# Kernel tuning notes

Hardware: AMD Instinct MI355X
Metric: run time of the kernel (lower is better)

Reference implementation:

```python
import jax, jax.numpy as jnp
import numpy as np

B, CIN, HID, COUT, D, L = 2, 32, 64, 32, 20, 3
D2 = 2 * D
C4, C2 = COUT // 4, COUT // 2


def _conv3(x, W, b):
    # dense stride-1 'SAME' conv == MinkowskiConvolution on occupied set (background is 0)
    y = jax.lax.conv_general_dilated(x, W, (1, 1, 1), 'SAME',
                                     dimension_numbers=('NCDHW', 'OIDHW', 'NCDHW'))
    return y + b[None, :, None, None, None]


def _up(x, W, b):
    # generative conv-transpose, kernel 2 stride 2: out[:, :, 2i+p, 2j+q, 2k+r] = sum_c W[c,:,p,q,r] x[:,c,i,j,k]
    y = jnp.einsum('bcxyz,cdpqr->bdxpyqzr', x, W)
    y = y.reshape(x.shape[0], W.shape[1], 2 * x.shape[2], 2 * x.shape[3], 2 * x.shape[4])
    return y + b[None, :, None, None, None]


def _forward(x_feat, x_occ, target_occ, W_up, b_up, W_conv, b_conv,
             blk_W00, blk_b00, blk_W01, blk_b01, blk_W10, blk_b10,
             blk_W11, blk_b11, blk_W12, blk_b12, W_cls, b_cls, adaptive, rho=1.0):
    b = x_feat.shape[0]
    # occupancy of upsampled coords: every input voxel spawns its 2x2x2 children
    occ_up = jnp.repeat(jnp.repeat(jnp.repeat(x_occ, 2, 1), 2, 2), 2, 3)  # [B,D2,D2,D2]
    m = occ_up[:, None].astype(x_feat.dtype)
    out = jax.nn.relu(_up(x_feat, W_up, b_up) * m)
    out = jax.nn.relu(_conv3(out, W_conv, b_conv) * m)
    # InceptionResNet blocks (PCGCv2 style): two branches, concat, residual add
    for i in range(L):
        o0 = jax.nn.relu(_conv3(out, blk_W00[i], blk_b00[i]) * m)
        o0 = _conv3(o0, blk_W01[i], blk_b01[i]) * m
        o1 = jax.nn.relu(_conv3(out, blk_W10[i], blk_b10[i]) * m)
        o1 = jax.nn.relu(_conv3(o1, blk_W11[i], blk_b11[i]) * m)
        o1 = _conv3(o1, blk_W12[i], blk_b12[i]) * m
        out = jnp.concatenate([o0, o1], axis=1) + out
    out_cls = _conv3(out, W_cls, b_cls) * m
    # get_target_by_sp_tensor: isin(out coords, target coords) -> dense mask intersection
    occ_b = occ_up.astype(bool)
    target = occ_b & target_occ.astype(bool)
    # keep mask (computed under no_grad in torch)
    cls = jax.lax.stop_gradient(out_cls[:, 0]).reshape(b, -1)
    occ_flat = occ_b.reshape(b, -1)
    if adaptive:
        vals = jnp.where(occ_flat, cls, -jnp.inf)
        t_cnt = target_occ.astype(bool).reshape(b, -1).sum(-1)
        k = jnp.minimum(occ_flat.sum(-1), (t_cnt.astype(jnp.float32) * rho).astype(jnp.int32))
        order = jnp.argsort(-vals, axis=-1)
        ranks = jnp.argsort(order, axis=-1)   # descending rank of each voxel
        keep = (ranks < k[:, None]) & occ_flat
    else:
        keep = (cls > 0) & occ_flat
    keep = keep.reshape(occ_b.shape)
    keep = keep | target  # training mode: keep += target
    out_pruned = out * keep[:, None].astype(out.dtype)
    return out_pruned, out_cls, target, keep


def setup_inputs() -> dict:
    key = jax.random.key(0)
    ks = jax.random.split(key, 12)
    s = 0.05
    occ = jax.random.randint(ks[0], (B, D, D, D), 0, 2).astype(jnp.int32)
    x_feat = jax.random.normal(ks[1], (B, CIN, D, D, D), jnp.float32) * occ[:, None].astype(jnp.float32)
    target_occ = jax.random.randint(ks[2], (B, D2, D2, D2), 0, 2).astype(jnp.int32)
    return {
        'x_feat': x_feat, 'x_occ': occ, 'target_occ': target_occ,
        'W_up': jax.random.normal(ks[3], (CIN, HID, 2, 2, 2), jnp.float32) * s,
        'b_up': jnp.zeros((HID,), jnp.float32),
        'W_conv': jax.random.normal(ks[4], (COUT, HID, 3, 3, 3), jnp.float32) * s,
        'b_conv': jnp.zeros((COUT,), jnp.float32),
        'blk_W00': jax.random.normal(ks[5], (L, C4, COUT, 3, 3, 3), jnp.float32) * s,
        'blk_b00': jnp.zeros((L, C4), jnp.float32),
        'blk_W01': jax.random.normal(ks[6], (L, C2, C4, 3, 3, 3), jnp.float32) * s,
        'blk_b01': jnp.zeros((L, C2), jnp.float32),
        'blk_W10': jax.random.normal(ks[7], (L, C4, COUT, 1, 1, 1), jnp.float32) * s,
        'blk_b10': jnp.zeros((L, C4), jnp.float32),
        'blk_W11': jax.random.normal(ks[8], (L, C4, C4, 3, 3, 3), jnp.float32) * s,
        'blk_b11': jnp.zeros((L, C4), jnp.float32),
        'blk_W12': jax.random.normal(ks[9], (L, C2, C4, 1, 1, 1), jnp.float32) * s,
        'blk_b12': jnp.zeros((L, C2), jnp.float32),
        'W_cls': jax.random.normal(ks[10], (1, COUT, 3, 3, 3), jnp.float32) * s,
        'b_cls': jnp.zeros((1,), jnp.float32),
        'adaptive': 1,
    }


def reference(x_feat, x_occ, target_occ, W_up, b_up, W_conv, b_conv,
              blk_W00, blk_b00, blk_W01, blk_b01, blk_W10, blk_b10,
              blk_W11, blk_b11, blk_W12, blk_b12, W_cls, b_cls, adaptive):
    return _forward(x_feat, x_occ, target_occ, W_up, b_up, W_conv, b_conv,
                    blk_W00, blk_b00, blk_W01, blk_b01, blk_W10, blk_b10,
                    blk_W11, blk_b11, blk_W12, blk_b12, W_cls, b_cls, adaptive)
```

## Files before the change

### kernel.cpp

```cpp
#include <hip/hip_runtime.h>
#include <hip/hip_bf16.h>

#define S3 64000
#define NB 2

constexpr int OFF_WUP   = 0;
constexpr int OFF_WCONV = 16384;
constexpr int OFF_W00   = 71680;
constexpr int OFF_W01   = 92416;
constexpr int OFF_W10   = 102784;
constexpr int OFF_W11   = 103552;
constexpr int OFF_W12   = 108736;
constexpr int OFF_ZERO  = 109120;
constexpr int OFF_WCLS  = 109184;
constexpr int NPACK     = 110048;

__device__ const int g_offtab[27] = {
  -1641, -1640, -1639, -1601, -1600, -1599, -1561, -1560, -1559,
    -41,   -40,   -39,    -1,     0,     1,    39,    40,    41,
   1559,  1560,  1561,  1599,  1600,  1601,  1639,  1640,  1641
};

__device__ __forceinline__ int occ_at(const int* __restrict__ x_occ, int b, int s) {
  int d2 = s % 40; int t = s / 40; int d1 = t % 40; int d0 = t / 40;
  return x_occ[b * 8000 + (d0 >> 1) * 400 + (d1 >> 1) * 20 + (d2 >> 1)] != 0;
}

__device__ __forceinline__ unsigned int f2key(float f) {
  unsigned int u = __float_as_uint(f);
  return (u & 0x80000000u) ? ~u : (u | 0x80000000u);
}

__device__ __forceinline__ unsigned int edge_mask27(int d0, int d1, int d2) {
  unsigned int m = 0;
  #pragma unroll
  for (int k0 = 0; k0 < 3; ++k0)
  #pragma unroll
  for (int k1 = 0; k1 < 3; ++k1)
  #pragma unroll
  for (int k2 = 0; k2 < 3; ++k2) {
    bool ok = (k0 == 0 ? (d0 > 0) : (k0 == 2 ? (d0 < 39) : true))
           && (k1 == 0 ? (d1 > 0) : (k1 == 2 ? (d1 < 39) : true))
           && (k2 == 0 ? (d2 > 0) : (k2 == 2 ? (d2 < 39) : true));
    if (ok) m |= 1u << ((k0 * 3 + k1) * 3 + k2);
  }
  return m;
}

__global__ __launch_bounds__(256)
void pack_all(const float* __restrict__ Wup, const float* __restrict__ Wconv,
              const float* __restrict__ W00, const float* __restrict__ W01,
              const float* __restrict__ W10, const float* __restrict__ W11,
              const float* __restrict__ W12, const float* __restrict__ Wcls,
              float* __restrict__ wp) {
  int i = blockIdx.x * 256 + threadIdx.x;
  if (i < 16384) {
    int tap = i >> 11, rem = i & 2047, c = rem >> 6, d = rem & 63;
    wp[OFF_WUP + i] = Wup[((c << 6) | d) * 8 + tap];
    return;
  }
  i -= 16384;
  if (i < 55296) {
    int tap = i >> 11, c = (i >> 5) & 63, co = i & 31;
    wp[OFF_WCONV + i] = Wconv[(co * 64 + c) * 27 + tap];
    return;
  }
  i -= 55296;
  if (i < 20736) {
    int blk = i / 6912, r = i - blk * 6912;
    int tap = r >> 8, c = (r >> 3) & 31, co = r & 7;
    wp[OFF_W00 + i] = W00[((blk * 8 + co) * 32 + c) * 27 + tap];
    return;
  }
  i -= 20736;
  if (i < 10368) {
    int blk = i / 3456, r = i - blk * 3456;
    int tap = r >> 7, c = (r >> 4) & 7, co = r & 15;
    wp[OFF_W01 + i] = W01[((blk * 16 + co) * 8 + c) * 27 + tap];
    return;
  }
  i -= 10368;
  if (i < 768) {
    int blk = i / 256, r = i - blk * 256;
    int c = r >> 3, co = r & 7;
    wp[OFF_W10 + i] = W10[(blk * 8 + co) * 32 + c];
    return;
  }
  i -= 768;
  if (i < 5184) {
    int blk = i / 1728, r = i - blk * 1728;
    int tap = r >> 6, c = (r >> 3) & 7, co = r & 7;
    wp[OFF_W11 + i] = W11[((blk * 8 + co) * 8 + c) * 27 + tap];
    return;
  }
  i -= 5184;
  if (i < 384) {
    int blk = i / 128, r = i - blk * 128;
    int c = r >> 4, co = r & 15;
    wp[OFF_W12 + i] = W12[(blk * 16 + co) * 8 + c];
    return;
  }
  i -= 384;
  if (i < 64) {
    wp[OFF_ZERO + i] = 0.f;
    return;
  }
  i -= 64;
  if (i < 864) {
    int tap = i / 32, c = i % 32;
    wp[OFF_WCLS + i] = Wcls[c * 27 + tap];
  }
}

__global__ __launch_bounds__(64)
void up_kernel(const float* __restrict__ xf, const float* __restrict__ wup,
               const float* __restrict__ bup, const int* __restrict__ x_occ,
               float* __restrict__ outA) {
  int pv = blockIdx.x * 64 + threadIdx.x;
  int b = pv / 8000, p = pv - b * 8000;
  int p2 = p % 20, t = p / 20, p1 = t % 20, p0 = t / 20;
  int tap = blockIdx.y;
  int O0 = 2 * p0 + (tap >> 2), O1 = 2 * p1 + ((tap >> 1) & 1), O2 = 2 * p2 + (tap & 1);
  int s = O0 * 1600 + O1 * 40 + O2;
  float* op = outA + ((size_t)b * S3 + s) * 64;
  int occ = x_occ[pv];
  float4 z4 = make_float4(0.f, 0.f, 0.f, 0.f);
  if (!occ) {
    #pragma unroll
    for (int i = 0; i < 16; ++i) ((float4*)op)[i] = z4;
    return;
  }
  float acc[64];
  #pragma unroll
  for (int d = 0; d < 64; ++d) acc[d] = bup[d];
  const float* xb = xf + (size_t)b * 32 * 8000 + p;
  const float* wt = wup + tap * 2048;
  #pragma unroll 1
  for (int c = 0; c < 32; ++c) {
    float v = xb[c * 8000];
    const float* w = wt + c * 64;
    #pragma unroll
    for (int d = 0; d < 64; ++d) acc[d] = fmaf(v, w[d], acc[d]);
  }
  #pragma unroll
  for (int i = 0; i < 16; ++i)
    ((float4*)op)[i] = make_float4(fmaxf(acc[4*i],0.f), fmaxf(acc[4*i+1],0.f),
                                   fmaxf(acc[4*i+2],0.f), fmaxf(acc[4*i+3],0.f));
}

template<int CIN, int COUT, int WS, bool RELU>
__global__ __launch_bounds__(256)
void conv3_cl(const float* __restrict__ in, const float* __restrict__ w,
              const float* __restrict__ bias, const int* __restrict__ x_occ,
              const float* __restrict__ zpage, float* __restrict__ out, int outc) {
  int tid = blockIdx.x * 256 + threadIdx.x;
  int b = tid / S3, s = tid - b * S3;
  int d2 = s % 40; int t = s / 40; int d1 = t % 40; int d0 = t / 40;
  int occ = x_occ[b * 8000 + (d0 >> 1) * 400 + (d1 >> 1) * 20 + (d2 >> 1)];
  int cb = blockIdx.y * COUT;
  float* op = out + (size_t)tid * outc + cb;
  float4 z4 = make_float4(0.f, 0.f, 0.f, 0.f);
  if (!occ) {
    #pragma unroll
    for (int i = 0; i < COUT / 4; ++i) ((float4*)op)[i] = z4;
    return;
  }
  const float* wb = w + cb;
  const float* bb = bias + cb;
  float acc[COUT];
  #pragma unroll
  for (int co = 0; co < COUT; ++co) acc[co] = bb[co];
  const float* inb = in + (size_t)tid * CIN;
  unsigned int m27 = edge_mask27(d0, d1, d2);
  #pragma unroll 1
  for (int tap = 0; tap < 27; ++tap) {
    const float* p = ((m27 >> tap) & 1) ? (inb + g_offtab[tap] * CIN) : zpage;
    const float* wt = wb + tap * CIN * WS;
    #pragma unroll
    for (int c4 = 0; c4 < CIN / 4; ++c4) {
      float4 v = ((const float4*)p)[c4];
      const float* wc = wt + c4 * 4 * WS;
      #pragma unroll
      for (int co = 0; co < COUT; ++co) acc[co] = fmaf(v.x, wc[co], acc[co]);
      #pragma unroll
      for (int co = 0; co < COUT; ++co) acc[co] = fmaf(v.y, wc[WS + co], acc[co]);
      #pragma unroll
      for (int co = 0; co < COUT; ++co) acc[co] = fmaf(v.z, wc[2 * WS + co], acc[co]);
      #pragma unroll
      for (int co = 0; co < COUT; ++co) acc[co] = fmaf(v.w, wc[3 * WS + co], acc[co]);
    }
  }
  #pragma unroll
  for (int co = 0; co < COUT; ++co) if (RELU) acc[co] = fmaxf(acc[co], 0.f);
  #pragma unroll
  for (int i = 0; i < COUT / 4; ++i)
    ((float4*)op)[i] = make_float4(acc[4*i], acc[4*i+1], acc[4*i+2], acc[4*i+3]);
}

__global__ __launch_bounds__(256)
void conv_k1(const float* __restrict__ in, const float* __restrict__ w3,
             const float* __restrict__ w1, const float* __restrict__ b3,
             const float* __restrict__ b1, const int* __restrict__ x_occ,
             const float* __restrict__ zpage, float* __restrict__ T0o,
             float* __restrict__ T1o) {
  int tid = blockIdx.x * 256 + threadIdx.x;
  int b = tid / S3, s = tid - b * S3;
  int d2 = s % 40; int t = s / 40; int d1 = t % 40; int d0 = t / 40;
  int occ = x_occ[b * 8000 + (d0 >> 1) * 400 + (d1 >> 1) * 20 + (d2 >> 1)];
  float* o0 = T0o + (size_t)tid * 8;
  float* o1 = T1o + (size_t)tid * 8;
  float4 z4 = make_float4(0.f, 0.f, 0.f, 0.f);
  if (!occ) {
    ((float4*)o0)[0] = z4; ((float4*)o0)[1] = z4;
    ((float4*)o1)[0] = z4; ((float4*)o1)[1] = z4;
    return;
  }
  float a0[8], a1[8];
  #pragma unroll
  for (int co = 0; co < 8; ++co) { a0[co] = b3[co]; a1[co] = b1[co]; }
  const float* inb = in + (size_t)tid * 32;
  #pragma unroll
  for (int c4 = 0; c4 < 8; ++c4) {
    float4 v = ((const float4*)inb)[c4];
    const float* wc = w1 + c4 * 4 * 8;
    #pragma unroll
    for (int co = 0; co < 8; ++co) a1[co] = fmaf(v.x, wc[co], a1[co]);
    #pragma unroll
    for (int co = 0; co < 8; ++co) a1[co] = fmaf(v.y, wc[8 + co], a1[co]);
    #pragma unroll
    for (int co = 0; co < 8; ++co) a1[co] = fmaf(v.z, wc[16 + co], a1[co]);
    #pragma unroll
    for (int co = 0; co < 8; ++co) a1[co] = fmaf(v.w, wc[24 + co], a1[co]);
  }
  unsigned int m27 = edge_mask27(d0, d1, d2);
  #pragma unroll 1
  for (int tap = 0; tap < 27; ++tap) {
    const float* p = ((m27 >> tap) & 1) ? (inb + g_offtab[tap] * 32) : zpage;
    const float* wt = w3 + tap * 32 * 8;
    #pragma unroll
    for (int c4 = 0; c4 < 8; ++c4) {
      float4 v = ((const float4*)p)[c4];
      const float* wc = wt + c4 * 4 * 8;
      #pragma unroll
      for (int co = 0; co < 8; ++co) a0[co] = fmaf(v.x, wc[co], a0[co]);
      #pragma unroll
      for (int co = 0; co < 8; ++co) a0[co] = fmaf(v.y, wc[8 + co], a0[co]);
      #pragma unroll
      for (int co = 0; co < 8; ++co) a0[co] = fmaf(v.z, wc[16 + co], a0[co]);
      #pragma unroll
      for (int co = 0; co < 8; ++co) a0[co] = fmaf(v.w, wc[24 + co], a0[co]);
    }
  }
  ((float4*)o0)[0] = make_float4(fmaxf(a0[0],0.f), fmaxf(a0[1],0.f), fmaxf(a0[2],0.f), fmaxf(a0[3],0.f));
  ((float4*)o0)[1] = make_float4(fmaxf(a0[4],0.f), fmaxf(a0[5],0.f), fmaxf(a0[6],0.f), fmaxf(a0[7],0.f));
  ((float4*)o1)[0] = make_float4(fmaxf(a1[0],0.f), fmaxf(a1[1],0.f), fmaxf(a1[2],0.f), fmaxf(a1[3],0.f));
  ((float4*)o1)[1] = make_float4(fmaxf(a1[4],0.f), fmaxf(a1[5],0.f), fmaxf(a1[6],0.f), fmaxf(a1[7],0.f));
}

__global__ __launch_bounds__(256)
void conv_k3(const float* __restrict__ t0, const float* __restrict__ t2,
             const float* __restrict__ resid, const float* __restrict__ w01,
             const float* __restrict__ w12, const float* __restrict__ bb01,
             const float* __restrict__ bb12, const int* __restrict__ x_occ,
             const float* __restrict__ zpage, float* __restrict__ nxt) {
  int tid = blockIdx.x * 256 + threadIdx.x;
  int b = tid / S3, s = tid - b * S3;
  int d2 = s % 40; int t = s / 40; int d1 = t % 40; int d0 = t / 40;
  int occ = x_occ[b * 8000 + (d0 >> 1) * 400 + (d1 >> 1) * 20 + (d2 >> 1)];
  float* op = nxt + (size_t)tid * 32;
  float4 z4 = make_float4(0.f, 0.f, 0.f, 0.f);
  if (!occ) {
    #pragma unroll
    for (int i = 0; i < 8; ++i) ((float4*)op)[i] = z4;
    return;
  }
  float a[32];
  #pragma unroll
  for (int co = 0; co < 16; ++co) { a[co] = bb01[co]; a[16 + co] = bb12[co]; }
  const float* t0b = t0 + (size_t)tid * 8;
  unsigned int m27 = edge_mask27(d0, d1, d2);
  #pragma unroll 1
  for (int tap = 0; tap < 27; ++tap) {
    const float* p = ((m27 >> tap) & 1) ? (t0b + g_offtab[tap] * 8) : zpage;
    const float* wt = w01 + tap * 8 * 16;
    #pragma unroll
    for (int c4 = 0; c4 < 2; ++c4) {
      float4 v = ((const float4*)p)[c4];
      const float* wc = wt + c4 * 4 * 16;
      #pragma unroll
      for (int co = 0; co < 16; ++co) a[co] = fmaf(v.x, wc[co], a[co]);
      #pragma unroll
      for (int co = 0; co < 16; ++co) a[co] = fmaf(v.y, wc[16 + co], a[co]);
      #pragma unroll
      for (int co = 0; co < 16; ++co) a[co] = fmaf(v.z, wc[32 + co], a[co]);
      #pragma unroll
      for (int co = 0; co < 16; ++co) a[co] = fmaf(v.w, wc[48 + co], a[co]);
    }
  }
  const float* t2b = t2 + (size_t)tid * 8;
  #pragma unroll
  for (int c4 = 0; c4 < 2; ++c4) {
    float4 v = ((const float4*)t2b)[c4];
    const float* wc = w12 + c4 * 4 * 16;
    #pragma unroll
    for (int co = 0; co < 16; ++co) a[16 + co] = fmaf(v.x, wc[co], a[16 + co]);
    #pragma unroll
    for (int co = 0; co < 16; ++co) a[16 + co] = fmaf(v.y, wc[16 + co], a[16 + co]);
    #pragma unroll
    for (int co = 0; co < 16; ++co) a[16 + co] = fmaf(v.z, wc[32 + co], a[16 + co]);
    #pragma unroll
    for (int co = 0; co < 16; ++co) a[16 + co] = fmaf(v.w, wc[48 + co], a[16 + co]);
  }
  const float* rb = resid + (size_t)tid * 32;
  #pragma unroll
  for (int i = 0; i < 8; ++i) {
    float4 r = ((const float4*)rb)[i];
    a[4*i] += r.x; a[4*i+1] += r.y; a[4*i+2] += r.z; a[4*i+3] += r.w;
  }
  #pragma unroll
  for (int i = 0; i < 8; ++i)
    ((float4*)op)[i] = make_float4(a[4*i], a[4*i+1], a[4*i+2], a[4*i+3]);
}

__global__ __launch_bounds__(256)
void cls_kernel(const float* __restrict__ in, const float* __restrict__ w,
                const float* __restrict__ bias, const int* __restrict__ x_occ,
                const float* __restrict__ zpage, float* __restrict__ CLSo) {
  int tid = blockIdx.x * 256 + threadIdx.x;
  int b = tid / S3, s = tid - b * S3;
  int d2 = s % 40; int t = s / 40; int d1 = t % 40; int d0 = t / 40;
  int occ = x_occ[b * 8000 + (d0 >> 1) * 400 + (d1 >> 1) * 20 + (d2 >> 1)];
  if (!occ) { CLSo[tid] = 0.f; return; }
  float acc = bias[0];
  const float* inb = in + (size_t)tid * 32;
  unsigned int m27 = edge_mask27(d0, d1, d2);
  #pragma unroll 1
  for (int tap = 0; tap < 27; ++tap) {
    const float* p = ((m27 >> tap) & 1) ? (inb + g_offtab[tap] * 32) : zpage;
    const float* wt = w + tap * 32;
    #pragma unroll
    for (int c4 = 0; c4 < 8; ++c4) {
      float4 v = ((const float4*)p)[c4];
      acc = fmaf(v.x, wt[4*c4], acc);
      acc = fmaf(v.y, wt[4*c4+1], acc);
      acc = fmaf(v.z, wt[4*c4+2], acc);
      acc = fmaf(v.w, wt[4*c4+3], acc);
    }
  }
  CLSo[tid] = acc;
}


__global__ __launch_bounds__(256)
void sel_zero(int* __restrict__ hist) {
  int i = blockIdx.x * 256 + threadIdx.x;
  int n = 3 * NB * 65536 + NB * 16;
  for (int j = i; j < n; j += 512 * 256) hist[j] = 0;
}

__global__ __launch_bounds__(256)
void sel_hist1(const float* __restrict__ cls, const int* __restrict__ x_occ,
               const int* __restrict__ tgt, unsigned int* __restrict__ key,
               int* __restrict__ hist, int* __restrict__ sel) {
  int tid = blockIdx.x * 256 + threadIdx.x;
  int b = tid / S3, s = tid - b * S3;
  int occ = occ_at(x_occ, b, s);
  int tg = tgt[tid] != 0;
  unsigned int kk = occ ? f2key(cls[tid]) : 0u;
  key[tid] = kk;
  if (occ) atomicAdd(&hist[b * 65536 + (kk >> 16)], 1);
  unsigned long long bo = __ballot(occ);
  unsigned long long bt = __ballot(tg);
  if ((threadIdx.x & 63) == 0) {
    atomicAdd(&sel[b * 16 + 0], (int)__popcll(bo));
    atomicAdd(&sel[b * 16 + 1], (int)__popcll(bt));
  }
}

__global__ __launch_bounds__(256)
void sel_hist2(const unsigned int* __restrict__ key, const int* __restrict__ x_occ,
               int* __restrict__ hist, const int* __restrict__ sel) {
  int tid = blockIdx.x * 256 + threadIdx.x;
  int b = tid / S3, s = tid - b * S3;
  int B1 = sel[b * 16 + 4];
  if (B1 < 0) return;
  if (!occ_at(x_occ, b, s)) return;
  unsigned int kk = key[tid];
  if ((int)(kk >> 16) == B1) atomicAdd(&hist[(NB + b) * 65536 + (kk & 0xFFFFu)], 1);
}

__global__ __launch_bounds__(256)
void sel_hist3(const unsigned int* __restrict__ key, const int* __restrict__ x_occ,
               int* __restrict__ hist, const int* __restrict__ sel) {
  int tid = blockIdx.x * 256 + threadIdx.x;
  int b = tid / S3, s = tid - b * S3;
  int B1 = sel[b * 16 + 4];
  if (B1 < 0) return;
  if (!occ_at(x_occ, b, s)) return;
  unsigned int k32 = ((unsigned)B1 << 16) | (unsigned)sel[b * 16 + 5];
  if (key[tid] == k32) atomicAdd(&hist[(2 * NB + b) * 65536 + (65535 - s)], 1);
}

__global__ __launch_bounds__(256)
void sel_scan(int* __restrict__ hist, int* __restrict__ sel,
              const int* __restrict__ adaptive_flag, int phase) {
  int b = blockIdx.x;
  int* sb = sel + b * 16;
  __shared__ int chunk[256];
  __shared__ int s_active, s_rank;
  int t = threadIdx.x;
  if (t == 0) {
    int active = 1;
    if (phase == 0) {
      int k = min(sb[0], sb[1]);
      sb[2] = k; sb[3] = k;
      if (!adaptive_flag[0] || k == 0) {
        sb[4] = -1000000;
        *(unsigned long long*)(sb + 6) = ~0ull;
        active = 0;
      }
    } else if (sb[4] == -1000000) {
      active = 0;
    }
    s_active = active; s_rank = sb[3];
  }
  __syncthreads();
  if (!s_active) return;
  const int* hb = hist + (phase * NB + b) * 65536;
  int sum = 0;
  #pragma unroll 4
  for (int v = 0; v < 256; ++v) sum += hb[t * 256 + v];
  chunk[t] = sum;
  __syncthreads();
  if (t == 0) {
    int r = s_rank, acc = 0, C = 0;
    for (int c = 255; c >= 0; --c) {
      if (acc + chunk[c] >= r) { C = c; r -= acc; break; }
      acc += chunk[c];
    }
    int B = C * 256;
    acc = 0;
    for (int v = 255; v >= 0; --v) {
      int h = hb[C * 256 + v];
      if (acc + h >= r) { B = C * 256 + v; r -= acc; break; }
      acc += h;
    }
    if (phase == 0)      { sb[4] = B; sb[3] = r; }
    else if (phase == 1) { sb[5] = B; sb[3] = r; }
    else {
      unsigned long long T = ((unsigned long long)sb[4] << 16) | (unsigned)sb[5];
      T = (T << 16) | (unsigned)B;
      *(unsigned long long*)(sb + 6) = T;
    }
  }
}

__global__ __launch_bounds__(256)
void emit_prune(const float* __restrict__ cls, const unsigned int* __restrict__ key,
                const int* __restrict__ x_occ, const int* __restrict__ tgt,
                const int* __restrict__ adaptive_flag, const int* __restrict__ sel,
                const float* __restrict__ cur, float* __restrict__ dout) {
  int tid = blockIdx.x * 256 + threadIdx.x;
  int b = tid / S3, s = tid - b * S3;
  int occ = occ_at(x_occ, b, s);
  int tg = occ && (tgt[tid] != 0);
  float c = cls[tid];
  bool kp;
  if (adaptive_flag[0]) {
    unsigned long long T = *(const unsigned long long*)(sel + b * 16 + 6);
    unsigned long long k48 = ((unsigned long long)key[tid] << 16) | (unsigned)(65535 - s);
    kp = occ && (k48 >= T);
  } else {
    kp = occ && (c > 0.f);
  }
  kp = kp || tg;
  float* tail = dout + (size_t)NB * 32 * S3;
  tail[tid] = c;
  tail[NB * S3 + tid] = tg ? 1.f : 0.f;
  tail[2 * NB * S3 + tid] = kp ? 1.f : 0.f;
  float sc = kp ? 1.f : 0.f;
  const float4* ip = (const float4*)(cur + (size_t)tid * 32);
  float* ob = dout + (size_t)b * 32 * S3 + s;
  #pragma unroll
  for (int i = 0; i < 8; ++i) {
    float4 q = ip[i];
    ob[(4 * i) * S3] = q.x * sc; ob[(4 * i + 1) * S3] = q.y * sc;
    ob[(4 * i + 2) * S3] = q.z * sc; ob[(4 * i + 3) * S3] = q.w * sc;
  }
}

extern "C" void kernel_launch(void* const* d_in, const int* in_sizes, int n_in,
                              void* d_out, int out_size, void* d_ws, size_t ws_size,
                              hipStream_t stream) {
  const float* x_feat    = (const float*)d_in[0];
  const int*   x_occ     = (const int*)d_in[1];
  const int*   target_oc = (const int*)d_in[2];
  const float* W_up   = (const float*)d_in[3];
  const float* b_up   = (const float*)d_in[4];
  const float* W_conv = (const float*)d_in[5];
  const float* b_conv = (const float*)d_in[6];
  const float* W00 = (const float*)d_in[7];
  const float* b00 = (const float*)d_in[8];
  const float* W01 = (const float*)d_in[9];
  const float* b01 = (const float*)d_in[10];
  const float* W10 = (const float*)d_in[11];
  const float* b10 = (const float*)d_in[12];
  const float* W11 = (const float*)d_in[13];
  const float* b11 = (const float*)d_in[14];
  const float* W12 = (const float*)d_in[15];
  const float* b12 = (const float*)d_in[16];
  const float* W_cls = (const float*)d_in[17];
  const float* b_cls = (const float*)d_in[18];
  const int*   adaptive = (const int*)d_in[19];

  float* ws = (float*)d_ws;
  float* wp = ws;
  float* zp = wp + OFF_ZERO;
  float* A  = ws + (1 << 17);
  float* B0 = A + (size_t)NB * S3 * 64;
  float* B1 = B0 + (size_t)NB * S3 * 32;
  float* T0 = A;
  float* T1 = T0 + (size_t)NB * S3 * 8;
  float* T2 = T1 + (size_t)NB * S3 * 8;
  float* CLS = T2 + (size_t)NB * S3 * 8;
  unsigned int* KEY = (unsigned int*)(CLS + (size_t)NB * S3);
  int* HIST = (int*)(KEY + (size_t)NB * S3);
  int* SEL  = HIST + 3 * NB * 65536;

  float* outf = (float*)d_out;

  pack_all<<<(NPACK + 255) / 256, 256, 0, stream>>>(W_up, W_conv, W00, W01, W10, W11, W12, W_cls, wp);
  up_kernel<<<dim3(250, 8), 64, 0, stream>>>(x_feat, wp + OFF_WUP, b_up, x_occ, A);
  conv3_cl<64, 16, 32, true><<<dim3(500, 2), 256, 0, stream>>>(A, wp + OFF_WCONV, b_conv, x_occ, zp, B0, 32);

  float* cur = B0;
  float* nxt = B1;
  for (int i = 0; i < 3; ++i) {
    conv_k1<<<500, 256, 0, stream>>>(cur, wp + OFF_W00 + i * 6912, wp + OFF_W10 + i * 256,
                                     b00 + i * 8, b10 + i * 8, x_occ, zp, T0, T1);
    conv3_cl<8, 8, 8, true><<<dim3(500, 1), 256, 0, stream>>>(T1, wp + OFF_W11 + i * 1728, b11 + i * 8,
                                                              x_occ, zp, T2, 8);
    conv_k3<<<500, 256, 0, stream>>>(T0, T2, cur, wp + OFF_W01 + i * 3456, wp + OFF_W12 + i * 128,
                                     b01 + i * 16, b12 + i * 16, x_occ, zp, nxt);
    float* tswap = cur; cur = nxt; nxt = tswap;
  }
  cls_kernel<<<500, 256, 0, stream>>>(cur, wp + OFF_WCLS, b_cls, x_occ, zp, CLS);

  sel_zero<<<512, 256, 0, stream>>>(HIST);
  sel_hist1<<<500, 256, 0, stream>>>(CLS, x_occ, target_oc, KEY, HIST, SEL);
  sel_scan<<<NB, 256, 0, stream>>>(HIST, SEL, adaptive, 0);
  sel_hist2<<<500, 256, 0, stream>>>(KEY, x_occ, HIST, SEL);
  sel_scan<<<NB, 256, 0, stream>>>(HIST, SEL, adaptive, 1);
  sel_hist3<<<500, 256, 0, stream>>>(KEY, x_occ, HIST, SEL);
  sel_scan<<<NB, 256, 0, stream>>>(HIST, SEL, adaptive, 2);
  emit_prune<<<500, 256, 0, stream>>>(CLS, KEY, x_occ, target_oc, adaptive, SEL, cur, outf);
}
```

Before: 676.5 us.

## Swizzle block IDs across XCDs and batch neighbor loads before FMAs in conv kernels

```diff
diff --git a/kernel.cpp b/kernel.cpp
--- a/kernel.cpp
+++ b/kernel.cpp
@@ -47,6 +47,12 @@
   return m;
 }
 
+__device__ __forceinline__ int swz_xcd(int bid, int G) {
+  int q = G >> 3, r = G & 7;
+  int x = bid & 7, i = bid >> 3;
+  return (x < r ? x * (q + 1) : r * (q + 1) + (x - r) * q) + i;
+}
+
 __global__ __launch_bounds__(256)
 void pack_all(const float* __restrict__ Wup, const float* __restrict__ Wconv,
               const float* __restrict__ W00, const float* __restrict__ W01,
@@ -101,10 +107,7 @@
     return;
   }
   i -= 384;
-  if (i < 64) {
-    wp[OFF_ZERO + i] = 0.f;
-    return;
-  }
+  if (i < 64) { wp[OFF_ZERO + i] = 0.f; return; }
   i -= 64;
   if (i < 864) {
     int tap = i / 32, c = i % 32;
@@ -148,16 +151,19 @@
                                    fmaxf(acc[4*i+2],0.f), fmaxf(acc[4*i+3],0.f));
 }
 
-template<int CIN, int COUT, int WS, bool RELU>
+template<int CIN, int COUT, int WS, bool RELU, int TAP_UNROLL>
 __global__ __launch_bounds__(256)
 void conv3_cl(const float* __restrict__ in, const float* __restrict__ w,
               const float* __restrict__ bias, const int* __restrict__ x_occ,
               const float* __restrict__ zpage, float* __restrict__ out, int outc) {
-  int tid = blockIdx.x * 256 + threadIdx.x;
+  int G = gridDim.x * gridDim.y;
+  int swl = swz_xcd(blockIdx.x + gridDim.x * blockIdx.y, G);
+  int xb = swl % gridDim.x, yb = swl / gridDim.x;
+  int tid = xb * 256 + threadIdx.x;
   int b = tid / S3, s = tid - b * S3;
   int d2 = s % 40; int t = s / 40; int d1 = t % 40; int d0 = t / 40;
   int occ = x_occ[b * 8000 + (d0 >> 1) * 400 + (d1 >> 1) * 20 + (d2 >> 1)];
-  int cb = blockIdx.y * COUT;
+  int cb = yb * COUT;
   float* op = out + (size_t)tid * outc + cb;
   float4 z4 = make_float4(0.f, 0.f, 0.f, 0.f);
   if (!occ) {
@@ -169,32 +175,35 @@
   const float* bb = bias + cb;
   float acc[COUT];
   #pragma unroll
-  for (int co = 0; co < COUT; ++co) acc[co] = bb[co];
+  for (int c = 0; c < COUT; ++c) acc[c] = bb[c];
   const float* inb = in + (size_t)tid * CIN;
   unsigned int m27 = edge_mask27(d0, d1, d2);
-  #pragma unroll 1
+  #pragma unroll TAP_UNROLL
   for (int tap = 0; tap < 27; ++tap) {
     const float* p = ((m27 >> tap) & 1) ? (inb + g_offtab[tap] * CIN) : zpage;
+    float4 vv[CIN / 4];
+    #pragma unroll
+    for (int c4 = 0; c4 < CIN / 4; ++c4) vv[c4] = ((const float4*)p)[c4];
     const float* wt = wb + tap * CIN * WS;
     #pragma unroll
     for (int c4 = 0; c4 < CIN / 4; ++c4) {
-      float4 v = ((const float4*)p)[c4];
+      float4 v = vv[c4];
       const float* wc = wt + c4 * 4 * WS;
       #pragma unroll
-      for (int co = 0; co < COUT; ++co) acc[co] = fmaf(v.x, wc[co], acc[co]);
-      #pragma unroll
-      for (int co = 0; co < COUT; ++co) acc[co] = fmaf(v.y, wc[WS + co], acc[co]);
-      #pragma unroll
-      for (int co = 0; co < COUT; ++co) acc[co] = fmaf(v.z, wc[2 * WS + co], acc[co]);
-      #pragma unroll
-      for (int co = 0; co < COUT; ++co) acc[co] = fmaf(v.w, wc[3 * WS + co], acc[co]);
-    }
-  }
-  #pragma unroll
-  for (int co = 0; co < COUT; ++co) if (RELU) acc[co] = fmaxf(acc[co], 0.f);
-  #pragma unroll
-  for (int i = 0; i < COUT / 4; ++i)
-    ((float4*)op)[i] = make_float4(acc[4*i], acc[4*i+1], acc[4*i+2], acc[4*i+3]);
+      for (int c = 0; c < COUT; ++c) acc[c] = fmaf(v.x, wc[c], acc[c]);
+      #pragma unroll
+      for (int c = 0; c < COUT; ++c) acc[c] = fmaf(v.y, wc[WS + c], acc[c]);
+      #pragma unroll
+      for (int c = 0; c < COUT; ++c) acc[c] = fmaf(v.z, wc[2 * WS + c], acc[c]);
+      #pragma unroll
+      for (int c = 0; c < COUT; ++c) acc[c] = fmaf(v.w, wc[3 * WS + c], acc[c]);
+    }
+  }
+  #pragma unroll
+  for (int c = 0; c < COUT; ++c) if (RELU) acc[c] = fmaxf(acc[c], 0.f);
+  #pragma unroll
+  for (int c = 0; c < COUT / 4; ++c)
+    ((float4*)op)[c] = make_float4(acc[4*c], acc[4*c+1], acc[4*c+2], acc[4*c+3]);
 }
 
 __global__ __launch_bounds__(256)
@@ -203,7 +212,8 @@
              const float* __restrict__ b1, const int* __restrict__ x_occ,
              const float* __restrict__ zpage, float* __restrict__ T0o,
              float* __restrict__ T1o) {
-  int tid = blockIdx.x * 256 + threadIdx.x;
+  int swl = swz_xcd(blockIdx.x, gridDim.x);
+  int tid = swl * 256 + threadIdx.x;
   int b = tid / S3, s = tid - b * S3;
   int d2 = s % 40; int t = s / 40; int d1 = t % 40; int d0 = t / 40;
   int occ = x_occ[b * 8000 + (d0 >> 1) * 400 + (d1 >> 1) * 20 + (d2 >> 1)];
@@ -219,28 +229,36 @@
   #pragma unroll
   for (int co = 0; co < 8; ++co) { a0[co] = b3[co]; a1[co] = b1[co]; }
   const float* inb = in + (size_t)tid * 32;
-  #pragma unroll
-  for (int c4 = 0; c4 < 8; ++c4) {
-    float4 v = ((const float4*)inb)[c4];
-    const float* wc = w1 + c4 * 4 * 8;
-    #pragma unroll
-    for (int co = 0; co < 8; ++co) a1[co] = fmaf(v.x, wc[co], a1[co]);
-    #pragma unroll
-    for (int co = 0; co < 8; ++co) a1[co] = fmaf(v.y, wc[8 + co], a1[co]);
-    #pragma unroll
-    for (int co = 0; co < 8; ++co) a1[co] = fmaf(v.z, wc[16 + co], a1[co]);
-    #pragma unroll
-    for (int co = 0; co < 8; ++co) a1[co] = fmaf(v.w, wc[24 + co], a1[co]);
+  {
+    float4 vv[8];
+    #pragma unroll
+    for (int c4 = 0; c4 < 8; ++c4) vv[c4] = ((const float4*)inb)[c4];
+    #pragma unroll
+    for (int c4 = 0; c4 < 8; ++c4) {
+      float4 v = vv[c4];
+      const float* wc = w1 + c4 * 32;
+      #pragma unroll
+      for (int co = 0; co < 8; ++co) a1[co] = fmaf(v.x, wc[co], a1[co]);
+      #pragma unroll
+      for (int co = 0; co < 8; ++co) a1[co] = fmaf(v.y, wc[8 + co], a1[co]);
+      #pragma unroll
+      for (int co = 0; co < 8; ++co) a1[co] = fmaf(v.z, wc[16 + co], a1[co]);
+      #pragma unroll
+      for (int co = 0; co < 8; ++co) a1[co] = fmaf(v.w, wc[24 + co], a1[co]);
+    }
   }
   unsigned int m27 = edge_mask27(d0, d1, d2);
   #pragma unroll 1
   for (int tap = 0; tap < 27; ++tap) {
     const float* p = ((m27 >> tap) & 1) ? (inb + g_offtab[tap] * 32) : zpage;
-    const float* wt = w3 + tap * 32 * 8;
+    float4 vv[8];
+    #pragma unroll
+    for (int c4 = 0; c4 < 8; ++c4) vv[c4] = ((const float4*)p)[c4];
+    const float* wt = w3 + tap * 256;
     #pragma unroll
     for (int c4 = 0; c4 < 8; ++c4) {
-      float4 v = ((const float4*)p)[c4];
-      const float* wc = wt + c4 * 4 * 8;
+      float4 v = vv[c4];
+      const float* wc = wt + c4 * 32;
       #pragma unroll
       for (int co = 0; co < 8; ++co) a0[co] = fmaf(v.x, wc[co], a0[co]);
       #pragma unroll
@@ -263,7 +281,8 @@
              const float* __restrict__ w12, const float* __restrict__ bb01,
              const float* __restrict__ bb12, const int* __restrict__ x_occ,
              const float* __restrict__ zpage, float* __restrict__ nxt) {
-  int tid = blockIdx.x * 256 + threadIdx.x;
+  int swl = swz_xcd(blockIdx.x, gridDim.x);
+  int tid = swl * 256 + threadIdx.x;
   int b = tid / S3, s = tid - b * S3;
   int d2 = s % 40; int t = s / 40; int d1 = t % 40; int d0 = t / 40;
   int occ = x_occ[b * 8000 + (d0 >> 1) * 400 + (d1 >> 1) * 20 + (d2 >> 1)];
@@ -279,14 +298,17 @@
   for (int co = 0; co < 16; ++co) { a[co] = bb01[co]; a[16 + co] = bb12[co]; }
   const float* t0b = t0 + (size_t)tid * 8;
   unsigned int m27 = edge_mask27(d0, d1, d2);
-  #pragma unroll 1
+  #pragma unroll 3
   for (int tap = 0; tap < 27; ++tap) {
     const float* p = ((m27 >> tap) & 1) ? (t0b + g_offtab[tap] * 8) : zpage;
-    const float* wt = w01 + tap * 8 * 16;
+    float4 vv[2];
+    vv[0] = ((const float4*)p)[0];
+    vv[1] = ((const float4*)p)[1];
+    const float* wt = w01 + tap * 128;
     #pragma unroll
     for (int c4 = 0; c4 < 2; ++c4) {
-      float4 v = ((const float4*)p)[c4];
-      const float* wc = wt + c4 * 4 * 16;
+      float4 v = vv[c4];
+      const float* wc = wt + c4 * 64;
       #pragma unroll
       for (int co = 0; co < 16; ++co) a[co] = fmaf(v.x, wc[co], a[co]);
       #pragma unroll
@@ -298,35 +320,41 @@
     }
   }
   const float* t2b = t2 + (size_t)tid * 8;
-  #pragma unroll
-  for (int c4 = 0; c4 < 2; ++c4) {
-    float4 v = ((const float4*)t2b)[c4];
-    const float* wc = w12 + c4 * 4 * 16;
-    #pragma unroll
-    for (int co = 0; co < 16; ++co) a[16 + co] = fmaf(v.x, wc[co], a[16 + co]);
-    #pragma unroll
-    for (int co = 0; co < 16; ++co) a[16 + co] = fmaf(v.y, wc[16 + co], a[16 + co]);
-    #pragma unroll
-    for (int co = 0; co < 16; ++co) a[16 + co] = fmaf(v.z, wc[32 + co], a[16 + co]);
-    #pragma unroll
-    for (int co = 0; co < 16; ++co) a[16 + co] = fmaf(v.w, wc[48 + co], a[16 + co]);
+  {
+    float4 vv[2];
+    vv[0] = ((const float4*)t2b)[0];
+    vv[1] = ((const float4*)t2b)[1];
+    #pragma unroll
+    for (int c4 = 0; c4 < 2; ++c4) {
+      float4 v = vv[c4];
+      const float* wc = w12 + c4 * 64;
+      #pragma unroll
+      for (int co = 0; co < 16; ++co) a[16 + co] = fmaf(v.x, wc[co], a[16 + co]);
+      #pragma unroll
+      for (int co = 0; co < 16; ++co) a[16 + co] = fmaf(v.y, wc[16 + co], a[16 + co]);
+      #pragma unroll
+      for (int co = 0; co < 16; ++co) a[16 + co] = fmaf(v.z, wc[32 + co], a[16 + co]);
+      #pragma unroll
+      for (int co = 0; co < 16; ++co) a[16 + co] = fmaf(v.w, wc[48 + co], a[16 + co]);
+    }
   }
   const float* rb = resid + (size_t)tid * 32;
   #pragma unroll
-  for (int i = 0; i < 8; ++i) {
-    float4 r = ((const float4*)rb)[i];
-    a[4*i] += r.x; a[4*i+1] += r.y; a[4*i+2] += r.z; a[4*i+3] += r.w;
-  }
-  #pragma unroll
-  for (int i = 0; i < 8; ++i)
-    ((float4*)op)[i] = make_float4(a[4*i], a[4*i+1], a[4*i+2], a[4*i+3]);
+  for (int q = 0; q < 8; ++q) {
+    float4 r = ((const float4*)rb)[q];
+    a[4*q] += r.x; a[4*q+1] += r.y; a[4*q+2] += r.z; a[4*q+3] += r.w;
+  }
+  #pragma unroll
+  for (int q = 0; q < 8; ++q)
+    ((float4*)op)[q] = make_float4(a[4*q], a[4*q+1], a[4*q+2], a[4*q+3]);
 }
 
 __global__ __launch_bounds__(256)
 void cls_kernel(const float* __restrict__ in, const float* __restrict__ w,
                 const float* __restrict__ bias, const int* __restrict__ x_occ,
                 const float* __restrict__ zpage, float* __restrict__ CLSo) {
-  int tid = blockIdx.x * 256 + threadIdx.x;
+  int swl = swz_xcd(blockIdx.x, gridDim.x);
+  int tid = swl * 256 + threadIdx.x;
   int b = tid / S3, s = tid - b * S3;
   int d2 = s % 40; int t = s / 40; int d1 = t % 40; int d0 = t / 40;
   int occ = x_occ[b * 8000 + (d0 >> 1) * 400 + (d1 >> 1) * 20 + (d2 >> 1)];
@@ -337,10 +365,13 @@
   #pragma unroll 1
   for (int tap = 0; tap < 27; ++tap) {
     const float* p = ((m27 >> tap) & 1) ? (inb + g_offtab[tap] * 32) : zpage;
+    float4 vv[8];
+    #pragma unroll
+    for (int c4 = 0; c4 < 8; ++c4) vv[c4] = ((const float4*)p)[c4];
     const float* wt = w + tap * 32;
     #pragma unroll
     for (int c4 = 0; c4 < 8; ++c4) {
-      float4 v = ((const float4*)p)[c4];
+      float4 v = vv[c4];
       acc = fmaf(v.x, wt[4*c4], acc);
       acc = fmaf(v.y, wt[4*c4+1], acc);
       acc = fmaf(v.z, wt[4*c4+2], acc);
@@ -349,7 +380,6 @@
   }
   CLSo[tid] = acc;
 }
-
 
 __global__ __launch_bounds__(256)
 void sel_zero(int* __restrict__ hist) {
@@ -531,15 +561,15 @@
 
   pack_all<<<(NPACK + 255) / 256, 256, 0, stream>>>(W_up, W_conv, W00, W01, W10, W11, W12, W_cls, wp);
   up_kernel<<<dim3(250, 8), 64, 0, stream>>>(x_feat, wp + OFF_WUP, b_up, x_occ, A);
-  conv3_cl<64, 16, 32, true><<<dim3(500, 2), 256, 0, stream>>>(A, wp + OFF_WCONV, b_conv, x_occ, zp, B0, 32);
+  conv3_cl<64, 16, 32, true, 1><<<dim3(500, 2), 256, 0, stream>>>(A, wp + OFF_WCONV, b_conv, x_occ, zp, B0, 32);
 
   float* cur = B0;
   float* nxt = B1;
   for (int i = 0; i < 3; ++i) {
     conv_k1<<<500, 256, 0, stream>>>(cur, wp + OFF_W00 + i * 6912, wp + OFF_W10 + i * 256,
                                      b00 + i * 8, b10 + i * 8, x_occ, zp, T0, T1);
-    conv3_cl<8, 8, 8, true><<<dim3(500, 1), 256, 0, stream>>>(T1, wp + OFF_W11 + i * 1728, b11 + i * 8,
-                                                              x_occ, zp, T2, 8);
+    conv3_cl<8, 8, 8, true, 3><<<dim3(500, 1), 256, 0, stream>>>(T1, wp + OFF_W11 + i * 1728, b11 + i * 8,
+                                                                 x_occ, zp, T2, 8);
     conv_k3<<<500, 256, 0, stream>>>(T0, T2, cur, wp + OFF_W01 + i * 3456, wp + OFF_W12 + i * 128,
                                      b01 + i * 16, b12 + i * 16, x_occ, zp, nxt);
     float* tswap = cur; cur = nxt; nxt = tswap;
```

After: 748.5 us. 1.11x slower.

## Fuse W11 conv into block tail kernel and widen big conv with XCD swizzle

Applied to the files above, without the earlier changes.

```diff
diff --git a/kernel.cpp b/kernel.cpp
--- a/kernel.cpp
+++ b/kernel.cpp
@@ -47,6 +47,12 @@
   return m;
 }
 
+__device__ __forceinline__ int swz_xcd(int bid, int G) {
+  int q = G >> 3, r = G & 7;
+  int x = bid & 7, i = bid >> 3;
+  return (x < r ? x * (q + 1) : r * (q + 1) + (x - r) * q) + i;
+}
+
 __global__ __launch_bounds__(256)
 void pack_all(const float* __restrict__ Wup, const float* __restrict__ Wconv,
               const float* __restrict__ W00, const float* __restrict__ W01,
@@ -101,10 +107,7 @@
     return;
   }
   i -= 384;
-  if (i < 64) {
-    wp[OFF_ZERO + i] = 0.f;
-    return;
-  }
+  if (i < 64) { wp[OFF_ZERO + i] = 0.f; return; }
   i -= 64;
   if (i < 864) {
     int tap = i / 32, c = i % 32;
@@ -148,53 +151,50 @@
                                    fmaxf(acc[4*i+2],0.f), fmaxf(acc[4*i+3],0.f));
 }
 
-template<int CIN, int COUT, int WS, bool RELU>
-__global__ __launch_bounds__(256)
-void conv3_cl(const float* __restrict__ in, const float* __restrict__ w,
+__global__ __launch_bounds__(256)
+void conv_big(const float* __restrict__ in, const float* __restrict__ w,
               const float* __restrict__ bias, const int* __restrict__ x_occ,
-              const float* __restrict__ zpage, float* __restrict__ out, int outc) {
-  int tid = blockIdx.x * 256 + threadIdx.x;
+              const float* __restrict__ zpage, float* __restrict__ out) {
+  int swl = swz_xcd(blockIdx.x, gridDim.x);
+  int tid = swl * 256 + threadIdx.x;
   int b = tid / S3, s = tid - b * S3;
   int d2 = s % 40; int t = s / 40; int d1 = t % 40; int d0 = t / 40;
   int occ = x_occ[b * 8000 + (d0 >> 1) * 400 + (d1 >> 1) * 20 + (d2 >> 1)];
-  int cb = blockIdx.y * COUT;
-  float* op = out + (size_t)tid * outc + cb;
+  float* op = out + (size_t)tid * 32;
   float4 z4 = make_float4(0.f, 0.f, 0.f, 0.f);
   if (!occ) {
     #pragma unroll
-    for (int i = 0; i < COUT / 4; ++i) ((float4*)op)[i] = z4;
-    return;
-  }
-  const float* wb = w + cb;
-  const float* bb = bias + cb;
-  float acc[COUT];
-  #pragma unroll
-  for (int co = 0; co < COUT; ++co) acc[co] = bb[co];
-  const float* inb = in + (size_t)tid * CIN;
+    for (int i = 0; i < 8; ++i) ((float4*)op)[i] = z4;
+    return;
+  }
+  float acc[32];
+  #pragma unroll
+  for (int c = 0; c < 32; ++c) acc[c] = bias[c];
+  const float* inb = in + (size_t)tid * 64;
   unsigned int m27 = edge_mask27(d0, d1, d2);
   #pragma unroll 1
   for (int tap = 0; tap < 27; ++tap) {
-    const float* p = ((m27 >> tap) & 1) ? (inb + g_offtab[tap] * CIN) : zpage;
-    const float* wt = wb + tap * CIN * WS;
-    #pragma unroll
-    for (int c4 = 0; c4 < CIN / 4; ++c4) {
+    const float* p = ((m27 >> tap) & 1) ? (inb + g_offtab[tap] * 64) : zpage;
+    const float* wt = w + tap * 64 * 32;
+    #pragma unroll
+    for (int c4 = 0; c4 < 16; ++c4) {
       float4 v = ((const float4*)p)[c4];
-      const float* wc = wt + c4 * 4 * WS;
-      #pragma unroll
-      for (int co = 0; co < COUT; ++co) acc[co] = fmaf(v.x, wc[co], acc[co]);
-      #pragma unroll
-      for (int co = 0; co < COUT; ++co) acc[co] = fmaf(v.y, wc[WS + co], acc[co]);
-      #pragma unroll
-      for (int co = 0; co < COUT; ++co) acc[co] = fmaf(v.z, wc[2 * WS + co], acc[co]);
-      #pragma unroll
-      for (int co = 0; co < COUT; ++co) acc[co] = fmaf(v.w, wc[3 * WS + co], acc[co]);
-    }
-  }
-  #pragma unroll
-  for (int co = 0; co < COUT; ++co) if (RELU) acc[co] = fmaxf(acc[co], 0.f);
-  #pragma unroll
-  for (int i = 0; i < COUT / 4; ++i)
-    ((float4*)op)[i] = make_float4(acc[4*i], acc[4*i+1], acc[4*i+2], acc[4*i+3]);
+      const float* wc = wt + c4 * 4 * 32;
+      #pragma unroll
+      for (int c = 0; c < 32; ++c) acc[c] = fmaf(v.x, wc[c], acc[c]);
+      #pragma unroll
+      for (int c = 0; c < 32; ++c) acc[c] = fmaf(v.y, wc[32 + c], acc[c]);
+      #pragma unroll
+      for (int c = 0; c < 32; ++c) acc[c] = fmaf(v.z, wc[64 + c], acc[c]);
+      #pragma unroll
+      for (int c = 0; c < 32; ++c) acc[c] = fmaf(v.w, wc[96 + c], acc[c]);
+    }
+  }
+  #pragma unroll
+  for (int c = 0; c < 32; ++c) acc[c] = fmaxf(acc[c], 0.f);
+  #pragma unroll
+  for (int c = 0; c < 8; ++c)
+    ((float4*)op)[c] = make_float4(acc[4*c], acc[4*c+1], acc[4*c+2], acc[4*c+3]);
 }
 
 __global__ __launch_bounds__(256)
@@ -258,11 +258,12 @@
 }
 
 __global__ __launch_bounds__(256)
-void conv_k3(const float* __restrict__ t0, const float* __restrict__ t2,
-             const float* __restrict__ resid, const float* __restrict__ w01,
-             const float* __restrict__ w12, const float* __restrict__ bb01,
-             const float* __restrict__ bb12, const int* __restrict__ x_occ,
-             const float* __restrict__ zpage, float* __restrict__ nxt) {
+void conv_k3f(const float* __restrict__ t0, const float* __restrict__ t1,
+              const float* __restrict__ resid, const float* __restrict__ w01,
+              const float* __restrict__ w11, const float* __restrict__ w12,
+              const float* __restrict__ bb01, const float* __restrict__ bb11,
+              const float* __restrict__ bb12, const int* __restrict__ x_occ,
+              const float* __restrict__ zpage, float* __restrict__ nxt) {
   int tid = blockIdx.x * 256 + threadIdx.x;
   int b = tid / S3, s = tid - b * S3;
   int d2 = s % 40; int t = s / 40; int d1 = t % 40; int d0 = t / 40;
@@ -274,19 +275,24 @@
     for (int i = 0; i < 8; ++i) ((float4*)op)[i] = z4;
     return;
   }
-  float a[32];
-  #pragma unroll
-  for (int co = 0; co < 16; ++co) { a[co] = bb01[co]; a[16 + co] = bb12[co]; }
+  float a[16], t2[8];
+  #pragma unroll
+  for (int co = 0; co < 16; ++co) a[co] = bb01[co];
+  #pragma unroll
+  for (int co = 0; co < 8; ++co) t2[co] = bb11[co];
   const float* t0b = t0 + (size_t)tid * 8;
+  const float* t1b = t1 + (size_t)tid * 8;
   unsigned int m27 = edge_mask27(d0, d1, d2);
   #pragma unroll 1
   for (int tap = 0; tap < 27; ++tap) {
-    const float* p = ((m27 >> tap) & 1) ? (t0b + g_offtab[tap] * 8) : zpage;
-    const float* wt = w01 + tap * 8 * 16;
+    bool ok = (m27 >> tap) & 1;
+    const float* p0 = ok ? (t0b + g_offtab[tap] * 8) : zpage;
+    const float* p1 = ok ? (t1b + g_offtab[tap] * 8) : zpage;
+    const float* wt0 = w01 + tap * 128;
     #pragma unroll
     for (int c4 = 0; c4 < 2; ++c4) {
-      float4 v = ((const float4*)p)[c4];
-      const float* wc = wt + c4 * 4 * 16;
+      float4 v = ((const float4*)p0)[c4];
+      const float* wc = wt0 + c4 * 64;
       #pragma unroll
       for (int co = 0; co < 16; ++co) a[co] = fmaf(v.x, wc[co], a[co]);
       #pragma unroll
@@ -296,30 +302,43 @@
       #pragma unroll
       for (int co = 0; co < 16; ++co) a[co] = fmaf(v.w, wc[48 + co], a[co]);
     }
-  }
-  const float* t2b = t2 + (size_t)tid * 8;
-  #pragma unroll
-  for (int c4 = 0; c4 < 2; ++c4) {
-    float4 v = ((const float4*)t2b)[c4];
-    const float* wc = w12 + c4 * 4 * 16;
-    #pragma unroll
-    for (int co = 0; co < 16; ++co) a[16 + co] = fmaf(v.x, wc[co], a[16 + co]);
-    #pragma unroll
-    for (int co = 0; co < 16; ++co) a[16 + co] = fmaf(v.y, wc[16 + co], a[16 + co]);
-    #pragma unroll
-    for (int co = 0; co < 16; ++co) a[16 + co] = fmaf(v.z, wc[32 + co], a[16 + co]);
-    #pragma unroll
-    for (int co = 0; co < 16; ++co) a[16 + co] = fmaf(v.w, wc[48 + co], a[16 + co]);
+    const float* wt1 = w11 + tap * 64;
+    #pragma unroll
+    for (int c4 = 0; c4 < 2; ++c4) {
+      float4 v = ((const float4*)p1)[c4];
+      const float* wc = wt1 + c4 * 32;
+      #pragma unroll
+      for (int co = 0; co < 8; ++co) t2[co] = fmaf(v.x, wc[co], t2[co]);
+      #pragma unroll
+      for (int co = 0; co < 8; ++co) t2[co] = fmaf(v.y, wc[8 + co], t2[co]);
+      #pragma unroll
+      for (int co = 0; co < 8; ++co) t2[co] = fmaf(v.z, wc[16 + co], t2[co]);
+      #pragma unroll
+      for (int co = 0; co < 8; ++co) t2[co] = fmaf(v.w, wc[24 + co], t2[co]);
+    }
+  }
+  #pragma unroll
+  for (int co = 0; co < 8; ++co) t2[co] = fmaxf(t2[co], 0.f);
+  float a1[16];
+  #pragma unroll
+  for (int co = 0; co < 16; ++co) a1[co] = bb12[co];
+  #pragma unroll
+  for (int c = 0; c < 8; ++c) {
+    #pragma unroll
+    for (int co = 0; co < 16; ++co) a1[co] = fmaf(t2[c], w12[c * 16 + co], a1[co]);
   }
   const float* rb = resid + (size_t)tid * 32;
-  #pragma unroll
-  for (int i = 0; i < 8; ++i) {
-    float4 r = ((const float4*)rb)[i];
-    a[4*i] += r.x; a[4*i+1] += r.y; a[4*i+2] += r.z; a[4*i+3] += r.w;
-  }
-  #pragma unroll
-  for (int i = 0; i < 8; ++i)
-    ((float4*)op)[i] = make_float4(a[4*i], a[4*i+1], a[4*i+2], a[4*i+3]);
+  float o[32];
+  #pragma unroll
+  for (int co = 0; co < 16; ++co) { o[co] = a[co]; o[16 + co] = a1[co]; }
+  #pragma unroll
+  for (int q = 0; q < 8; ++q) {
+    float4 r = ((const float4*)rb)[q];
+    o[4*q] += r.x; o[4*q+1] += r.y; o[4*q+2] += r.z; o[4*q+3] += r.w;
+  }
+  #pragma unroll
+  for (int q = 0; q < 8; ++q)
+    ((float4*)op)[q] = make_float4(o[4*q], o[4*q+1], o[4*q+2], o[4*q+3]);
 }
 
 __global__ __launch_bounds__(256)
@@ -349,7 +368,6 @@
   }
   CLSo[tid] = acc;
 }
-
 
 __global__ __launch_bounds__(256)
 void sel_zero(int* __restrict__ hist) {
@@ -521,8 +539,7 @@
   float* B1 = B0 + (size_t)NB * S3 * 32;
   float* T0 = A;
   float* T1 = T0 + (size_t)NB * S3 * 8;
-  float* T2 = T1 + (size_t)NB * S3 * 8;
-  float* CLS = T2 + (size_t)NB * S3 * 8;
+  float* CLS = T1 + (size_t)NB * S3 * 8;
   unsigned int* KEY = (unsigned int*)(CLS + (size_t)NB * S3);
   int* HIST = (int*)(KEY + (size_t)NB * S3);
   int* SEL  = HIST + 3 * NB * 65536;
@@ -531,17 +548,16 @@
 
   pack_all<<<(NPACK + 255) / 256, 256, 0, stream>>>(W_up, W_conv, W00, W01, W10, W11, W12, W_cls, wp);
   up_kernel<<<dim3(250, 8), 64, 0, stream>>>(x_feat, wp + OFF_WUP, b_up, x_occ, A);
-  conv3_cl<64, 16, 32, true><<<dim3(500, 2), 256, 0, stream>>>(A, wp + OFF_WCONV, b_conv, x_occ, zp, B0, 32);
+  conv_big<<<500, 256, 0, stream>>>(A, wp + OFF_WCONV, b_conv, x_occ, zp, B0);
 
   float* cur = B0;
   float* nxt = B1;
   for (int i = 0; i < 3; ++i) {
     conv_k1<<<500, 256, 0, stream>>>(cur, wp + OFF_W00 + i * 6912, wp + OFF_W10 + i * 256,
                                      b00 + i * 8, b10 + i * 8, x_occ, zp, T0, T1);
-    conv3_cl<8, 8, 8, true><<<dim3(500, 1), 256, 0, stream>>>(T1, wp + OFF_W11 + i * 1728, b11 + i * 8,
-                                                              x_occ, zp, T2, 8);
-    conv_k3<<<500, 256, 0, stream>>>(T0, T2, cur, wp + OFF_W01 + i * 3456, wp + OFF_W12 + i * 128,
-                                     b01 + i * 16, b12 + i * 16, x_occ, zp, nxt);
+    conv_k3f<<<500, 256, 0, stream>>>(T0, T1, cur, wp + OFF_W01 + i * 3456, wp + OFF_W11 + i * 1728,
+                                      wp + OFF_W12 + i * 128, b01 + i * 16, b11 + i * 8, b12 + i * 16,
+                                      x_occ, zp, nxt);
     float* tswap = cur; cur = nxt; nxt = tswap;
   }
   cls_kernel<<<500, 256, 0, stream>>>(cur, wp + OFF_WCLS, b_cls, x_occ, zp, CLS);
```

Result: slower. 787.6 us (+16.4%).
